# Kernel tuning notes

Measured on AMD Instinct MI355X. Metric: run time of the kernel, lower is better.

Reference implementation:

```python
import jax, jax.numpy as jnp
import numpy as np

N_FEATS = 128
N_NODES = 100000
N_EDGES = 1000000
NUM_SEGMENTS = 4096


def setup_inputs() -> dict:
    key = jax.random.key(0)
    ks = jax.random.split(key, 10)
    glorot = lambda k, shape: jax.random.uniform(
        k, shape, dtype=jnp.float32,
        minval=-1.0, maxval=1.0) * np.sqrt(6.0 / (shape[0] + shape[1]))
    x_j = jax.random.normal(ks[0], (N_NODES, N_FEATS), dtype=jnp.float32)
    x_i = jax.random.normal(ks[1], (N_NODES, N_FEATS), dtype=jnp.float32)
    edge_index = jax.random.randint(ks[2], (2, N_EDGES), 0, N_NODES)
    edge_index_batch = jnp.sort(jax.random.randint(ks[3], (N_EDGES,), 0, NUM_SEGMENTS))
    w_j = glorot(ks[4], (N_FEATS, N_FEATS))
    w_i = glorot(ks[5], (N_FEATS, N_FEATS))
    bias = jnp.zeros((N_FEATS,), dtype=jnp.float32)
    prelu_w = jnp.array(0.25, dtype=jnp.float32)  # nn.PReLU default init
    # nn.Linear(out_feats, 1) default init: U(-1/sqrt(fan_in), 1/sqrt(fan_in))
    lim = 1.0 / np.sqrt(N_FEATS)
    mlp_W = jax.random.uniform(ks[6], (N_FEATS, 1), dtype=jnp.float32, minval=-lim, maxval=lim)
    mlp_b = jax.random.uniform(ks[7], (1,), dtype=jnp.float32, minval=-lim, maxval=lim)
    return {"x_j": x_j, "x_i": x_i, "edge_index": edge_index,
            "edge_index_batch": edge_index_batch, "w_j": w_j, "w_i": w_i,
            "bias": bias, "prelu_w": prelu_w, "mlp_W": mlp_W, "mlp_b": mlp_b}


def reference(x_j, x_i, edge_index, edge_index_batch, w_j, w_i, bias, prelu_w, mlp_W, mlp_b):
    # project node features: [N, F]
    xi = x_i @ w_i
    xj = x_j @ w_j
    # gather endpoints per edge and fuse bias add: [E, F]
    h = xj[edge_index[0]] + xi[edge_index[1]] + bias
    # PReLU (single shared slope) then Linear(F, 1) -> [E]
    h = jnp.where(h >= 0, h, prelu_w * h)
    alpha = (h @ mlp_W).reshape(-1) + mlp_b[0]
    # per-graph segmented softmax (PyG torch_geometric.utils.softmax)
    seg_max = jax.ops.segment_max(alpha, edge_index_batch, num_segments=NUM_SEGMENTS)
    e = jnp.exp(alpha - seg_max[edge_index_batch])
    seg_sum = jax.ops.segment_sum(e, edge_index_batch, num_segments=NUM_SEGMENTS)
    return e / (seg_sum[edge_index_batch] + 1e-16)
```

## Files before the change

### kernel.cpp

```cpp
#include <hip/hip_runtime.h>
#include <hip/hip_fp16.h>
#include <float.h>

#define NSEG 4096
#define CAP 2048

typedef __attribute__((ext_vector_type(8))) _Float16 half8;
typedef __attribute__((ext_vector_type(2))) _Float16 h2v;
typedef __attribute__((ext_vector_type(4))) float f32x4;

__global__ void seg_bounds(const int* __restrict__ batch, int* __restrict__ segs, int E) {
  int b = blockIdx.x * blockDim.x + threadIdx.x;
  if (b > NSEG) return;
  int lo = 0, hi = E;
  while (lo < hi) { int mid = (lo + hi) >> 1; if (batch[mid] < b) lo = mid + 1; else hi = mid; }
  segs[b] = lo;
}

__global__ __launch_bounds__(256) void pack_w(
    const float* __restrict__ Wj, const float* __restrict__ Wi,
    __half* __restrict__ Wpk) {
  int tid = blockIdx.x * blockDim.x + threadIdx.x;
  for (int idx = tid; idx < 2 * 4 * 8 * 64 * 8; idx += gridDim.x * blockDim.x) {
    int r     = idx & 7;
    int l     = (idx >> 3) & 63;
    int nt    = (idx >> 9) & 7;
    int kt    = (idx >> 12) & 3;
    int which = idx >> 14;
    const float* W = which ? Wi : Wj;
    int k = kt * 32 + (l >> 4) * 8 + r;
    int n = nt * 16 + (l & 15);
    float v = W[k * 128 + n];
    __half hi = __float2half(v);
    __half lo = __float2half(v - __half2float(hi));
    size_t base = ((size_t)which * 32 + (size_t)(kt * 8 + nt)) * 1024;
    Wpk[base + l * 8 + r]       = hi;
    Wpk[base + 512 + l * 8 + r] = lo;
  }
}

__global__ __launch_bounds__(256) void proj_mfma(
    const float* __restrict__ Xj, const float* __restrict__ Xi,
    const float* __restrict__ bias, const __half* __restrict__ Wpk,
    __half* __restrict__ Yj, __half* __restrict__ Yi, int nrows) {
  const int which = blockIdx.y;
  const float* X = which ? Xi : Xj;
  __half* Y = which ? Yi : Yj;
  const _Float16* WpkB = (const _Float16*)Wpk + (size_t)which * 32768;

  __shared__ _Float16 Wlds[2][8192];

  const int tid  = threadIdx.x;
  const int wid  = tid >> 6;
  const int lane = tid & 63;
  const int lr   = lane & 15;
  const int lg   = lane >> 4;

  const long row0 = (long)blockIdx.x * 128 + wid * 32;
  long r0 = row0 + lr;
  long r1 = row0 + 16 + lr;
  const float* p0 = X + (r0 < nrows ? r0 : 0) * 128 + lg * 8;
  const float* p1 = X + (r1 < nrows ? r1 : 0) * 128 + lg * 8;

  {
    const float4* s_ = (const float4*)(WpkB);
    float4* d_ = (float4*)Wlds[0];
    d_[tid]       = s_[tid];
    d_[256 + tid] = s_[256 + tid];
    d_[512 + tid] = s_[512 + tid];
    d_[768 + tid] = s_[768 + tid];
  }
  float4 xa0 = *(const float4*)(p0);
  float4 xb0 = *(const float4*)(p0 + 4);
  float4 xa1 = *(const float4*)(p1);
  float4 xb1 = *(const float4*)(p1 + 4);

  __syncthreads();

  f32x4 acc[2][8] = {};

#define CVT1(dsth, dstl, idx, val)                                   \
  { float v_ = (val); _Float16 h_ = (_Float16)v_;                    \
    dsth[idx] = h_; dstl[idx] = (_Float16)(v_ - (float)h_); }
#define CVT8(dsth, dstl, v0, v1)                                     \
  CVT1(dsth, dstl, 0, (v0).x) CVT1(dsth, dstl, 1, (v0).y)            \
  CVT1(dsth, dstl, 2, (v0).z) CVT1(dsth, dstl, 3, (v0).w)            \
  CVT1(dsth, dstl, 4, (v1).x) CVT1(dsth, dstl, 5, (v1).y)            \
  CVT1(dsth, dstl, 6, (v1).z) CVT1(dsth, dstl, 7, (v1).w)

#define MFMA(a, b, c) __builtin_amdgcn_mfma_f32_16x16x32_f16((a), (b), (c), 0, 0, 0)

#define KT_STEP(kt, LAST)                                                \
  {                                                                      \
    float4 sw0, sw1, sw2, sw3;                                           \
    if (!(LAST)) {                                                       \
      const float4* s_ = (const float4*)(WpkB + ((kt) + 1) * 8192);      \
      sw0 = s_[tid];                                                     \
      sw1 = s_[256 + tid];                                               \
      sw2 = s_[512 + tid];                                               \
      sw3 = s_[768 + tid];                                               \
    }                                                                    \
    half8 xh0, xl0, xh1, xl1;                                            \
    CVT8(xh0, xl0, xa0, xb0);                                            \
    CVT8(xh1, xl1, xa1, xb1);                                            \
    if (!(LAST)) {                                                       \
      xa0 = *(const float4*)(p0 + ((kt) + 1) * 32);                      \
      xb0 = *(const float4*)(p0 + ((kt) + 1) * 32 + 4);                  \
      xa1 = *(const float4*)(p1 + ((kt) + 1) * 32);                      \
      xb1 = *(const float4*)(p1 + ((kt) + 1) * 32 + 4);                  \
      float4* d_ = (float4*)Wlds[((kt) + 1) & 1];                        \
      d_[tid]       = sw0;                                               \
      d_[256 + tid] = sw1;                                               \
      d_[512 + tid] = sw2;                                               \
      d_[768 + tid] = sw3;                                               \
    }                                                                    \
    _Pragma("unroll")                                                    \
    for (int nt = 0; nt < 8; ++nt) {                                     \
      const _Float16* f = &Wlds[(kt) & 1][nt * 1024 + lane * 8];         \
      half8 wh = *(const half8*)(f);                                     \
      half8 wl = *(const half8*)(f + 512);                               \
      acc[0][nt] = MFMA(wh, xh0, acc[0][nt]);                            \
      acc[1][nt] = MFMA(wh, xh1, acc[1][nt]);                            \
      acc[0][nt] = MFMA(wh, xl0, acc[0][nt]);                            \
      acc[1][nt] = MFMA(wh, xl1, acc[1][nt]);                            \
      acc[0][nt] = MFMA(wl, xh0, acc[0][nt]);                            \
      acc[1][nt] = MFMA(wl, xh1, acc[1][nt]);                            \
    }                                                                    \
    if (!(LAST)) __syncthreads();                                        \
  }

  KT_STEP(0, 0)
  KT_STEP(1, 0)
  KT_STEP(2, 0)
  KT_STEP(3, 1)

#undef KT_STEP
#undef MFMA
#undef CVT8
#undef CVT1

  #pragma unroll
  for (int mt = 0; mt < 2; ++mt) {
    long row = row0 + mt * 16 + lr;
    if (row < nrows) {
      __half* yr = Y + row * 128;
      #pragma unroll
      for (int nt = 0; nt < 8; ++nt) {
        float4 bv = make_float4(0.f, 0.f, 0.f, 0.f);
        if (which) bv = *(const float4*)(bias + nt * 16 + lg * 4);
        __half2 v01 = __floats2half2_rn(acc[mt][nt][0] + bv.x, acc[mt][nt][1] + bv.y);
        __half2 v23 = __floats2half2_rn(acc[mt][nt][2] + bv.z, acc[mt][nt][3] + bv.w);
        uint2 u;
        u.x = *(unsigned int*)&v01;
        u.y = *(unsigned int*)&v23;
        *(uint2*)(yr + nt * 16 + lg * 4) = u;
      }
    }
  }
}

__global__ __launch_bounds__(256) void seg_softmax(
    const __half* __restrict__ xjp, const __half* __restrict__ xip,
    const int* __restrict__ ei, const int* __restrict__ segs,
    const float* __restrict__ mlpW, const float* __restrict__ prelu_w,
    const float* __restrict__ mlp_b, float* __restrict__ out, int E) {
  const int start = segs[blockIdx.x];
  const int end = segs[blockIdx.x + 1];
  const int cnt = end - start;
  if (cnt <= 0) return;

  __shared__ float aS[CAP];
  __shared__ float red[8];

  const int tid = threadIdx.x;
  const int lane = tid & 63;
  const int wid = tid >> 6;
  const int g   = tid >> 4;
  const int ql  = tid & 15;

  const float4 w0 = *(const float4*)(mlpW + ql * 8);
  const float4 w1 = *(const float4*)(mlpW + ql * 8 + 4);
  const float pw = prelu_w[0];
  const float mb = mlp_b[0];
  const bool useLds = (cnt <= CAP);

  const uint4* XJ = (const uint4*)xjp;
  const uint4* XI = (const uint4*)xip;
  const h2v pwv = { (_Float16)pw, (_Float16)pw };
  const h2v zv  = { (_Float16)0.f, (_Float16)0.f };

  for (int e0 = start + g * 4; e0 < end; e0 += 64) {
    const int eB = e0 + 1, eC = e0 + 2, eD = e0 + 3;
    const bool vB = (eB < end), vC = (eC < end), vD = (eD < end);
    int sA = ei[e0],            dA = ei[E + e0];
    int sB = vB ? ei[eB] : sA,  dB = vB ? ei[E + eB] : dA;
    int sC = vC ? ei[eC] : sA,  dC = vC ? ei[E + eC] : dA;
    int sD = vD ? ei[eD] : sA,  dD = vD ? ei[E + eD] : dA;

    uint4 aA = XJ[(size_t)sA * 16 + ql], bA = XI[(size_t)dA * 16 + ql];
    uint4 aB = XJ[(size_t)sB * 16 + ql], bB = XI[(size_t)dB * 16 + ql];
    uint4 aC = XJ[(size_t)sC * 16 + ql], bC = XI[(size_t)dC * 16 + ql];
    uint4 aD = XJ[(size_t)sD * 16 + ql], bD = XI[(size_t)dD * 16 + ql];

    float pA, pB, pC, pD;
#define EALPHA(av, bv, p)                                                   \
    {                                                                       \
      h2v h0 = *(h2v*)&(av).x + *(h2v*)&(bv).x;                             \
      h2v h1 = *(h2v*)&(av).y + *(h2v*)&(bv).y;                             \
      h2v h2 = *(h2v*)&(av).z + *(h2v*)&(bv).z;                             \
      h2v h3 = *(h2v*)&(av).w + *(h2v*)&(bv).w;                             \
      h0 = __builtin_elementwise_max(h0, zv)                                \
         + pwv * __builtin_elementwise_min(h0, zv);                         \
      h1 = __builtin_elementwise_max(h1, zv)                                \
         + pwv * __builtin_elementwise_min(h1, zv);                         \
      h2 = __builtin_elementwise_max(h2, zv)                                \
         + pwv * __builtin_elementwise_min(h2, zv);                         \
      h3 = __builtin_elementwise_max(h3, zv)                                \
         + pwv * __builtin_elementwise_min(h3, zv);                         \
      p = (float)h0.x * w0.x;                                               \
      p = fmaf((float)h0.y, w0.y, p); p = fmaf((float)h1.x, w0.z, p);       \
      p = fmaf((float)h1.y, w0.w, p); p = fmaf((float)h2.x, w1.x, p);       \
      p = fmaf((float)h2.y, w1.y, p); p = fmaf((float)h3.x, w1.z, p);       \
      p = fmaf((float)h3.y, w1.w, p);                                       \
    }
    EALPHA(aA, bA, pA);
    EALPHA(aB, bB, pB);
    EALPHA(aC, bC, pC);
    EALPHA(aD, bD, pD);
#undef EALPHA

    #pragma unroll
    for (int off = 1; off < 16; off <<= 1) {
      pA += __shfl_xor(pA, off, 64);
      pB += __shfl_xor(pB, off, 64);
      pC += __shfl_xor(pC, off, 64);
      pD += __shfl_xor(pD, off, 64);
    }
    if (ql == 0) {
      if (useLds) {
        aS[e0 - start] = pA + mb;
        if (vB) aS[eB - start] = pB + mb;
        if (vC) aS[eC - start] = pC + mb;
        if (vD) aS[eD - start] = pD + mb;
      } else {
        out[e0] = pA + mb;
        if (vB) out[eB] = pB + mb;
        if (vC) out[eC] = pC + mb;
        if (vD) out[eD] = pD + mb;
      }
    }
  }
  __syncthreads();

  float m = -FLT_MAX;
  if (useLds) { for (int i = tid; i < cnt; i += 256) m = fmaxf(m, aS[i]); }
  else        { for (int i = tid; i < cnt; i += 256) m = fmaxf(m, out[start + i]); }
  #pragma unroll
  for (int off = 1; off < 64; off <<= 1) m = fmaxf(m, __shfl_xor(m, off, 64));
  if (lane == 0) red[wid] = m;
  __syncthreads();
  m = fmaxf(fmaxf(red[0], red[1]), fmaxf(red[2], red[3]));

  float s = 0.f;
  if (useLds) {
    for (int i = tid; i < cnt; i += 256) { float x = expf(aS[i] - m); aS[i] = x; s += x; }
  } else {
    for (int i = tid; i < cnt; i += 256) { float x = expf(out[start + i] - m); out[start + i] = x; s += x; }
  }
  #pragma unroll
  for (int off = 1; off < 64; off <<= 1) s += __shfl_xor(s, off, 64);
  if (lane == 0) red[4 + wid] = s;
  __syncthreads();
  s = (red[4] + red[5]) + (red[6] + red[7]);

  const float inv = 1.0f / (s + 1e-16f);
  if (useLds) { for (int i = tid; i < cnt; i += 256) out[start + i] = aS[i] * inv; }
  else        { for (int i = tid; i < cnt; i += 256) out[start + i] *= inv; }
}

extern "C" void kernel_launch(void* const* d_in, const int* in_sizes, int n_in,
                              void* d_out, int out_size, void* d_ws, size_t ws_size,
                              hipStream_t stream) {
  const float* x_j      = (const float*)d_in[0];
  const float* x_i      = (const float*)d_in[1];
  const int*   edge_idx = (const int*)d_in[2];
  const int*   batch    = (const int*)d_in[3];
  const float* w_j      = (const float*)d_in[4];
  const float* w_i      = (const float*)d_in[5];
  const float* bias     = (const float*)d_in[6];
  const float* prelu_w  = (const float*)d_in[7];
  const float* mlp_W    = (const float*)d_in[8];
  const float* mlp_b    = (const float*)d_in[9];
  const int nnodes = in_sizes[0] / 128;
  const int E = in_sizes[3];

  __half* Wpk = (__half*)d_ws;
  __half* xjp = Wpk + 65536;
  __half* xip = xjp + (size_t)nnodes * 128;
  int* segs   = (int*)(xip + (size_t)nnodes * 128);

  hipLaunchKernelGGL(seg_bounds, dim3((NSEG + 1 + 255) / 256), dim3(256), 0, stream,
                     batch, segs, E);

  hipLaunchKernelGGL(pack_w, dim3(32), dim3(256), 0, stream, w_j, w_i, Wpk);

  int gblocks = (nnodes + 127) / 128;
  hipLaunchKernelGGL(proj_mfma, dim3(gblocks, 2), dim3(256), 0, stream,
                     x_j, x_i, bias, Wpk, xjp, xip, nnodes);

  hipLaunchKernelGGL(seg_softmax, dim3(NSEG), dim3(256), 0, stream,
                     xjp, xip, edge_idx, segs, mlp_W, prelu_w, mlp_b,
                     (float*)d_out, E);
}
```

Measured before the change: 252.7 us.

## Merge setup kernels, halve rows per projection block, deepen X prefetch

Fuses the segment-bounds search and the weight-packing kernel into one launch, which removes one kernel launch. The projection kernel now gives each wave 16 rows instead of 32, so twice as many blocks run and more waves are in flight. It also prefetches X two k-steps ahead and moves the LDS weight store after the MFMA loop. In exchange, each block reloads the packed weights into LDS for half as many rows, which doubles total weight traffic.

After: 243.0 us. -3.9%, faster.

```diff
diff --git a/kernel.cpp b/kernel.cpp
--- a/kernel.cpp
+++ b/kernel.cpp
@@ -9,33 +9,35 @@
 typedef __attribute__((ext_vector_type(2))) _Float16 h2v;
 typedef __attribute__((ext_vector_type(4))) float f32x4;
 
-__global__ void seg_bounds(const int* __restrict__ batch, int* __restrict__ segs, int E) {
-  int b = blockIdx.x * blockDim.x + threadIdx.x;
-  if (b > NSEG) return;
-  int lo = 0, hi = E;
-  while (lo < hi) { int mid = (lo + hi) >> 1; if (batch[mid] < b) lo = mid + 1; else hi = mid; }
-  segs[b] = lo;
-}
-
-__global__ __launch_bounds__(256) void pack_w(
+__global__ __launch_bounds__(256) void setup(
+    const int* __restrict__ batch, int* __restrict__ segs, int E,
     const float* __restrict__ Wj, const float* __restrict__ Wi,
     __half* __restrict__ Wpk) {
-  int tid = blockIdx.x * blockDim.x + threadIdx.x;
-  for (int idx = tid; idx < 2 * 4 * 8 * 64 * 8; idx += gridDim.x * blockDim.x) {
-    int r     = idx & 7;
-    int l     = (idx >> 3) & 63;
-    int nt    = (idx >> 9) & 7;
-    int kt    = (idx >> 12) & 3;
-    int which = idx >> 14;
-    const float* W = which ? Wi : Wj;
-    int k = kt * 32 + (l >> 4) * 8 + r;
-    int n = nt * 16 + (l & 15);
-    float v = W[k * 128 + n];
-    __half hi = __float2half(v);
-    __half lo = __float2half(v - __half2float(hi));
-    size_t base = ((size_t)which * 32 + (size_t)(kt * 8 + nt)) * 1024;
-    Wpk[base + l * 8 + r]       = hi;
-    Wpk[base + 512 + l * 8 + r] = lo;
+  const int bid = blockIdx.x;
+  if (bid < 17) {
+    int b = bid * 256 + threadIdx.x;
+    if (b > NSEG) return;
+    int lo = 0, hi = E;
+    while (lo < hi) { int mid = (lo + hi) >> 1; if (batch[mid] < b) lo = mid + 1; else hi = mid; }
+    segs[b] = lo;
+  } else {
+    int tid = (bid - 17) * 256 + threadIdx.x;
+    for (int idx = tid; idx < 2 * 4 * 8 * 64 * 8; idx += 32 * 256) {
+      int r     = idx & 7;
+      int l     = (idx >> 3) & 63;
+      int nt    = (idx >> 9) & 7;
+      int kt    = (idx >> 12) & 3;
+      int which = idx >> 14;
+      const float* W = which ? Wi : Wj;
+      int k = kt * 32 + (l >> 4) * 8 + r;
+      int n = nt * 16 + (l & 15);
+      float v = W[k * 128 + n];
+      __half hi = __float2half(v);
+      __half lo = __float2half(v - __half2float(hi));
+      size_t base = ((size_t)which * 32 + (size_t)(kt * 8 + nt)) * 1024;
+      Wpk[base + l * 8 + r]       = hi;
+      Wpk[base + 512 + l * 8 + r] = lo;
+    }
   }
 }
 
@@ -56,11 +58,9 @@
   const int lr   = lane & 15;
   const int lg   = lane >> 4;
 
-  const long row0 = (long)blockIdx.x * 128 + wid * 32;
+  const long row0 = (long)blockIdx.x * 64 + wid * 16;
   long r0 = row0 + lr;
-  long r1 = row0 + 16 + lr;
   const float* p0 = X + (r0 < nrows ? r0 : 0) * 128 + lg * 8;
-  const float* p1 = X + (r1 < nrows ? r1 : 0) * 128 + lg * 8;
 
   {
     const float4* s_ = (const float4*)(WpkB);
@@ -70,14 +70,14 @@
     d_[512 + tid] = s_[512 + tid];
     d_[768 + tid] = s_[768 + tid];
   }
-  float4 xa0 = *(const float4*)(p0);
-  float4 xb0 = *(const float4*)(p0 + 4);
-  float4 xa1 = *(const float4*)(p1);
-  float4 xb1 = *(const float4*)(p1 + 4);
+  float4 xa = *(const float4*)(p0);
+  float4 xb = *(const float4*)(p0 + 4);
+  float4 na = *(const float4*)(p0 + 32);
+  float4 nb = *(const float4*)(p0 + 36);
 
   __syncthreads();
 
-  f32x4 acc[2][8] = {};
+  f32x4 acc[8] = {};
 
 #define CVT1(dsth, dstl, idx, val)                                   \
   { float v_ = (val); _Float16 h_ = (_Float16)v_;                    \
@@ -90,71 +90,65 @@
 
 #define MFMA(a, b, c) __builtin_amdgcn_mfma_f32_16x16x32_f16((a), (b), (c), 0, 0, 0)
 
-#define KT_STEP(kt, LAST)                                                \
+#define KT_STEP(kt, HASN1, HASN2)                                        \
   {                                                                      \
     float4 sw0, sw1, sw2, sw3;                                           \
-    if (!(LAST)) {                                                       \
+    if (HASN1) {                                                         \
       const float4* s_ = (const float4*)(WpkB + ((kt) + 1) * 8192);      \
       sw0 = s_[tid];                                                     \
       sw1 = s_[256 + tid];                                               \
       sw2 = s_[512 + tid];                                               \
       sw3 = s_[768 + tid];                                               \
     }                                                                    \
-    half8 xh0, xl0, xh1, xl1;                                            \
-    CVT8(xh0, xl0, xa0, xb0);                                            \
-    CVT8(xh1, xl1, xa1, xb1);                                            \
-    if (!(LAST)) {                                                       \
-      xa0 = *(const float4*)(p0 + ((kt) + 1) * 32);                      \
-      xb0 = *(const float4*)(p0 + ((kt) + 1) * 32 + 4);                  \
-      xa1 = *(const float4*)(p1 + ((kt) + 1) * 32);                      \
-      xb1 = *(const float4*)(p1 + ((kt) + 1) * 32 + 4);                  \
-      float4* d_ = (float4*)Wlds[((kt) + 1) & 1];                        \
-      d_[tid]       = sw0;                                               \
-      d_[256 + tid] = sw1;                                               \
-      d_[512 + tid] = sw2;                                               \
-      d_[768 + tid] = sw3;                                               \
+    half8 xh, xl;                                                        \
+    CVT8(xh, xl, xa, xb);                                                \
+    if (HASN1) { xa = na; xb = nb; }                                     \
+    if (HASN2) {                                                         \
+      na = *(const float4*)(p0 + ((kt) + 2) * 32);                       \
+      nb = *(const float4*)(p0 + ((kt) + 2) * 32 + 4);                   \
     }                                                                    \
     _Pragma("unroll")                                                    \
     for (int nt = 0; nt < 8; ++nt) {                                     \
       const _Float16* f = &Wlds[(kt) & 1][nt * 1024 + lane * 8];         \
       half8 wh = *(const half8*)(f);                                     \
       half8 wl = *(const half8*)(f + 512);                               \
-      acc[0][nt] = MFMA(wh, xh0, acc[0][nt]);                            \
-      acc[1][nt] = MFMA(wh, xh1, acc[1][nt]);                            \
-      acc[0][nt] = MFMA(wh, xl0, acc[0][nt]);                            \
-      acc[1][nt] = MFMA(wh, xl1, acc[1][nt]);                            \
-      acc[0][nt] = MFMA(wl, xh0, acc[0][nt]);                            \
-      acc[1][nt] = MFMA(wl, xh1, acc[1][nt]);                            \
+      acc[nt] = MFMA(wh, xh, acc[nt]);                                   \
+      acc[nt] = MFMA(wh, xl, acc[nt]);                                   \
+      acc[nt] = MFMA(wl, xh, acc[nt]);                                   \
     }                                                                    \
-    if (!(LAST)) __syncthreads();                                        \
-  }
-
-  KT_STEP(0, 0)
-  KT_STEP(1, 0)
-  KT_STEP(2, 0)
-  KT_STEP(3, 1)
+    if (HASN1) {                                                         \
+      float4* d_ = (float4*)Wlds[((kt) + 1) & 1];                        \
+      d_[tid]       = sw0;                                               \
+      d_[256 + tid] = sw1;                                               \
+      d_[512 + tid] = sw2;                                               \
+      d_[768 + tid] = sw3;                                               \
+      __syncthreads();                                                   \
+    }                                                                    \
+  }
+
+  KT_STEP(0, 1, 1)
+  KT_STEP(1, 1, 1)
+  KT_STEP(2, 1, 0)
+  KT_STEP(3, 0, 0)
 
 #undef KT_STEP
 #undef MFMA
 #undef CVT8
 #undef CVT1
 
-  #pragma unroll
-  for (int mt = 0; mt < 2; ++mt) {
-    long row = row0 + mt * 16 + lr;
-    if (row < nrows) {
-      __half* yr = Y + row * 128;
-      #pragma unroll
-      for (int nt = 0; nt < 8; ++nt) {
-        float4 bv = make_float4(0.f, 0.f, 0.f, 0.f);
-        if (which) bv = *(const float4*)(bias + nt * 16 + lg * 4);
-        __half2 v01 = __floats2half2_rn(acc[mt][nt][0] + bv.x, acc[mt][nt][1] + bv.y);
-        __half2 v23 = __floats2half2_rn(acc[mt][nt][2] + bv.z, acc[mt][nt][3] + bv.w);
-        uint2 u;
-        u.x = *(unsigned int*)&v01;
-        u.y = *(unsigned int*)&v23;
-        *(uint2*)(yr + nt * 16 + lg * 4) = u;
-      }
+  long row = row0 + lr;
+  if (row < nrows) {
+    __half* yr = Y + row * 128;
+    #pragma unroll
+    for (int nt = 0; nt < 8; ++nt) {
+      float4 bv = make_float4(0.f, 0.f, 0.f, 0.f);
+      if (which) bv = *(const float4*)(bias + nt * 16 + lg * 4);
+      __half2 v01 = __floats2half2_rn(acc[nt][0] + bv.x, acc[nt][1] + bv.y);
+      __half2 v23 = __floats2half2_rn(acc[nt][2] + bv.z, acc[nt][3] + bv.w);
+      uint2 u;
+      u.x = *(unsigned int*)&v01;
+      u.y = *(unsigned int*)&v23;
+      *(uint2*)(yr + nt * 16 + lg * 4) = u;
     }
   }
 }
@@ -299,12 +293,10 @@
   __half* xip = xjp + (size_t)nnodes * 128;
   int* segs   = (int*)(xip + (size_t)nnodes * 128);
 
-  hipLaunchKernelGGL(seg_bounds, dim3((NSEG + 1 + 255) / 256), dim3(256), 0, stream,
-                     batch, segs, E);
-
-  hipLaunchKernelGGL(pack_w, dim3(32), dim3(256), 0, stream, w_j, w_i, Wpk);
-
-  int gblocks = (nnodes + 127) / 128;
+  hipLaunchKernelGGL(setup, dim3(49), dim3(256), 0, stream,
+                     batch, segs, E, w_j, w_i, Wpk);
+
+  int gblocks = (nnodes + 63) / 64;
   hipLaunchKernelGGL(proj_mfma, dim3(gblocks, 2), dim3(256), 0, stream,
                      x_j, x_i, bias, Wpk, xjp, xip, nnodes);
 
```
